# Performance work log

Measured on AMD Instinct MI355X. Metric: run time of the kernel, lower is better.

The kernel has to match this reference:

```python
import jax, jax.numpy as jnp
import numpy as np
from jax import lax

B = 512        # batch
SPEC = 300     # spectral bands / num_patches
DIM = 64
DEPTH = 5
HEADS = 4
DIM_HEAD = 16
MLP = 8
NCLS = 16
SCALE = DIM_HEAD ** -0.5


def setup_inputs() -> dict:
    key = jax.random.key(0)
    ks = jax.random.split(key, 16)
    s = 0.02
    d = {}
    d["input_tensor"] = jax.random.normal(ks[0], (B, 1, 5, 5, SPEC), jnp.float32)
    # SSE block: Conv3d(1,1,(1,1,300)) == contraction over spectral dim
    d["sse_w"] = jax.random.normal(ks[1], (SPEC,), jnp.float32) * s
    d["sse_b"] = jnp.zeros((1,), jnp.float32)
    # 3D CNN branch
    d["conv1_w"] = jax.random.normal(ks[2], (16, 1, 3, 3, 7), jnp.float32) * s
    d["conv1_b"] = jnp.zeros((16,), jnp.float32)
    d["conv2_w"] = jax.random.normal(ks[3], (32, 16, 3, 3, 3), jnp.float32) * s
    d["conv2_b"] = jnp.zeros((32,), jnp.float32)
    d["dense1_w"] = jax.random.normal(ks[4], (64, 9344), jnp.float32) * s
    d["dense1_b"] = jnp.zeros((64,), jnp.float32)
    # patch embedding + tokens
    d["patch_w"] = jax.random.normal(ks[5], (DIM, 25), jnp.float32) * s
    d["patch_b"] = jnp.zeros((DIM,), jnp.float32)
    d["cls_token"] = jax.random.normal(ks[6], (1, 1, DIM), jnp.float32)
    d["pos_emb"] = jax.random.normal(ks[7], (1, SPEC + 1, DIM), jnp.float32)
    # transformer layers (stacked over depth)
    d["ln1_g"] = jnp.ones((DEPTH, DIM), jnp.float32)
    d["ln1_b"] = jnp.zeros((DEPTH, DIM), jnp.float32)
    d["qkv_w"] = jax.random.normal(ks[8], (DEPTH, 3 * HEADS * DIM_HEAD, DIM), jnp.float32) * s
    d["attn_out_w"] = jax.random.normal(ks[9], (DEPTH, DIM, HEADS * DIM_HEAD), jnp.float32) * s
    d["attn_out_b"] = jnp.zeros((DEPTH, DIM), jnp.float32)
    d["ln2_g"] = jnp.ones((DEPTH, DIM), jnp.float32)
    d["ln2_b"] = jnp.zeros((DEPTH, DIM), jnp.float32)
    d["ff1_w"] = jax.random.normal(ks[10], (DEPTH, MLP, DIM), jnp.float32) * s
    d["ff1_b"] = jnp.zeros((DEPTH, MLP), jnp.float32)
    d["ff2_w"] = jax.random.normal(ks[11], (DEPTH, DIM, MLP), jnp.float32) * s
    d["ff2_b"] = jnp.zeros((DEPTH, DIM), jnp.float32)
    # head: LayerNorm(2*dim) + Linear(2*dim, num_classes)
    d["head_ln_g"] = jnp.ones((2 * DIM,), jnp.float32)
    d["head_ln_b"] = jnp.zeros((2 * DIM,), jnp.float32)
    d["head_w"] = jax.random.normal(ks[12], (NCLS, 2 * DIM), jnp.float32) * s
    d["head_b"] = jnp.zeros((NCLS,), jnp.float32)
    return d


def _ln(x, g, b, eps=1e-5):
    m = jnp.mean(x, -1, keepdims=True)
    v = jnp.mean((x - m) ** 2, -1, keepdims=True)
    return (x - m) * lax.rsqrt(v + eps) * g + b


def reference(input_tensor, sse_w, sse_b, conv1_w, conv1_b, conv2_w, conv2_b,
              dense1_w, dense1_b, patch_w, patch_b, cls_token, pos_emb,
              ln1_g, ln1_b, qkv_w, attn_out_w, attn_out_b, ln2_g, ln2_b,
              ff1_w, ff1_b, ff2_w, ff2_b, head_ln_g, head_ln_b, head_w, head_b):
    xin = input_tensor  # [B,1,5,5,300]
    # Spatial SE: Conv3d(1,1,(1,1,300)) -> sigmoid -> gate
    sq = jax.nn.sigmoid(jnp.einsum('bihwc,c->bhw', xin, sse_w)[:, None, :, :, None] + sse_b[0])
    xin = xin * sq

    # ---- 3D CNN branch ----
    dn = ('NCDHW', 'OIDHW', 'NCDHW')
    h = lax.conv_general_dilated(xin, conv1_w, (1, 1, 1), 'VALID', dimension_numbers=dn)
    h = jax.nn.relu(h + conv1_b[None, :, None, None, None])          # [B,16,3,3,294]
    h = lax.conv_general_dilated(h, conv2_w, (1, 1, 1), 'VALID', dimension_numbers=dn)
    h = jax.nn.relu(h + conv2_b[None, :, None, None, None])          # [B,32,1,1,292]
    y = h.reshape(h.shape[0], -1) @ dense1_w.T + dense1_b            # [B,64]

    # ---- SpectralFormer branch ----
    b = xin.shape[0]
    # torch .view(b, 1*300, 5*5) on contiguous [B,1,5,5,300]: pure C-order reshape
    x = xin.reshape(b, SPEC, 25)
    x = x @ patch_w.T + patch_b                                      # [B,300,64]
    cls = jnp.broadcast_to(cls_token, (b, 1, DIM))
    x = jnp.concatenate([cls, x], axis=1) + pos_emb[:, :SPEC + 1]    # [B,301,64]

    for i in range(DEPTH):
        # attention (residual + prenorm)
        xn = _ln(x, ln1_g[i], ln1_b[i])
        qkv = xn @ qkv_w[i].T                                        # [B,301,192]
        q, k, v = jnp.split(qkv, 3, axis=-1)
        def heads(t):
            return t.reshape(b, SPEC + 1, HEADS, DIM_HEAD).transpose(0, 2, 1, 3)
        q, k, v = heads(q), heads(k), heads(v)                       # [B,H,301,16]
        dots = jnp.einsum('bhid,bhjd->bhij', q, k) * SCALE
        attn = jax.nn.softmax(dots, axis=-1)
        o = jnp.einsum('bhij,bhjd->bhid', attn, v)
        o = o.transpose(0, 2, 1, 3).reshape(b, SPEC + 1, HEADS * DIM_HEAD)
        x = o @ attn_out_w[i].T + attn_out_b[i] + x
        # feedforward (residual + prenorm)
        xn = _ln(x, ln2_g[i], ln2_b[i])
        hid = jax.nn.gelu(xn @ ff1_w[i].T + ff1_b[i], approximate=False)
        x = hid @ ff2_w[i].T + ff2_b[i] + x

    cls_out = x[:, 0]                                                # [B,64]
    z = jnp.concatenate([cls_out, y], axis=-1)                       # [B,128]
    z = _ln(z, head_ln_g, head_ln_b)
    return z @ head_w.T + head_b                                     # [B,16]
```

## Files before the change

### kernel.cpp

```cpp
#include <hip/hip_runtime.h>
#include <cmath>

#define NB 512
#define SEQ 301
#define QSCALE 0.36067376022f

using f32x4  = __attribute__((ext_vector_type(4))) float;
using s16x4  = __attribute__((ext_vector_type(4))) short;
using s16x8  = __attribute__((ext_vector_type(8))) short;

#if __has_builtin(__builtin_amdgcn_exp2f)
#define EX2(x) __builtin_amdgcn_exp2f(x)
#else
#define EX2(x) exp2f(x)
#endif

__device__ __forceinline__ unsigned short f2bf(float f) {
  unsigned int u = __builtin_bit_cast(unsigned int, f);
  u += 0x7fffu + ((u >> 16) & 1u);
  return (unsigned short)(u >> 16);
}

__device__ __forceinline__ unsigned int pkbf(float lo, float hi) {
  unsigned int ulo = __builtin_bit_cast(unsigned int, lo) + 0x8000u;
  unsigned int uhi = __builtin_bit_cast(unsigned int, hi) + 0x8000u;
  return __builtin_amdgcn_perm(uhi, ulo, 0x07060302u);
}

__device__ __forceinline__ s16x4 pk4f(float a, float b, float c, float d) {
  uint2 u = make_uint2(pkbf(a, b), pkbf(c, d));
  return __builtin_bit_cast(s16x4, u);
}

__device__ __forceinline__ s16x4 pk4(float4 v) {
  return pk4f(v.x, v.y, v.z, v.w);
}

__device__ __forceinline__ f32x4 mm16(s16x4 a, s16x4 b, f32x4 c) {
  return __builtin_amdgcn_mfma_f32_16x16x16bf16_1k(a, b, c, 0, 0, 0);
}

__device__ __forceinline__ f32x4 mm32(s16x8 a, s16x8 b, f32x4 c) {
  return __builtin_amdgcn_mfma_f32_16x16x32_bf16(a, b, c, 0, 0, 0);
}

__device__ __forceinline__ s16x8 cat8(s16x4 a, s16x4 b) {
  return __builtin_shufflevector(a, b, 0, 1, 2, 3, 4, 5, 6, 7);
}

__device__ __forceinline__ float gelu_f(float a) {
  float z = fabsf(a) * 0.70710678f;
  float t = 1.f / (1.f + 0.3275911f * z);
  float poly = t*(0.254829592f + t*(-0.284496736f + t*(1.421413741f +
               t*(-1.453152027f + t*1.061405429f))));
  float e = EX2(-z*z*1.44269504f);
  float erfa = 1.f - poly*e;
  float erfz = copysignf(erfa, a);
  return 0.5f*a*(1.f + erfz);
}

__global__ __launch_bounds__(256) void k_prep(const float* __restrict__ w2c,
    unsigned short* __restrict__ wt2g) {
  int i = blockIdx.x*256 + threadIdx.x;
  if (i >= 96*148) return;
  int row = i/148, k = i - row*148;
  int kw_ = row >> 5, o2 = row & 31;
  unsigned short v = 0;
  if (k < 144) {
    int ci = k/9, r_ = k - ci*9;
    v = f2bf(w2c[o2*432 + ci*27 + r_*3 + kw_]);
  }
  wt2g[i] = v;
}

__global__ __launch_bounds__(256) void k_prep2(const float* __restrict__ pw,
    unsigned short* __restrict__ pwt) {
  int i = blockIdx.x*256 + threadIdx.x;
  if (i >= 64*32) return;
  int d = i >> 5, k = i & 31;
  pwt[i] = (k < 25) ? f2bf(pw[d*25 + k]) : (unsigned short)0;
}

__global__ __launch_bounds__(64) void k_sse(const float* __restrict__ xin,
    const float* __restrict__ sw, const float* __restrict__ sb, float* __restrict__ xs) {
  int blk = blockIdx.x; int b = blk / 25, p = blk % 25; int lane = threadIdx.x;
  const float* src = xin + (size_t)b*7500 + p*300;
  float s = 0.f;
  for (int c = lane; c < 300; c += 64) s += src[c]*sw[c];
  #pragma unroll
  for (int o = 32; o > 0; o >>= 1) s += __shfl_down(s, o, 64);
  s = __shfl(s, 0, 64);
  float sq = 1.f/(1.f + __expf(-(s + sb[0])));
  float* dst = xs + (size_t)b*7500 + p*300;
  for (int c = lane; c < 300; c += 64) dst[c] = src[c]*sq;
}

__global__ __launch_bounds__(256) void k_conv12(const float* __restrict__ xs,
    const float* __restrict__ w1c, const float* __restrict__ b1c,
    const unsigned short* __restrict__ wt2g, const float* __restrict__ b2c,
    float* __restrict__ c2) {
  int blk = blockIdx.x; int b = blk >> 2; int chunk = blk & 3;
  int w0 = chunk*73;
  int tid = threadIdx.x;
  int lane = tid & 63, wv = tid >> 6;
  int lm = lane & 15, lq = lane >> 4;
  __shared__ unsigned short xss[32*88];
  __shared__ unsigned short c1s[84*148];
  __shared__ alignas(8) unsigned short wt_s[96*148];

  const float* src = xs + (size_t)b*7500;
  for (int i = tid; i < 2025; i += 256) {
    int p = i/81, c = i - p*81;
    xss[p*88 + c] = f2bf(src[p*300 + w0 + c]);
  }
  for (int i = tid; i < 7*88; i += 256) xss[25*88 + i] = 0;
  for (int i = tid; i < 25*7; i += 256) { int p = i/7, c = 81 + i%7; xss[p*88 + c] = 0; }
  for (int i = tid; i < 9*148; i += 256) c1s[75*148 + i] = 0;
  {
    const uint2* wsrc = (const uint2*)wt2g;
    uint2* wdst = (uint2*)wt_s;
    for (int i = tid; i < 3552; i += 256) wdst[i] = wsrc[i];
  }

  s16x4 Af[4]; int P[4][4]; float bv[4];
  #pragma unroll
  for (int r = 0; r < 4; ++r) bv[r] = b1c[lq*4 + r];
  #pragma unroll
  for (int kc = 0; kc < 4; ++kc) {
    short e[4];
    #pragma unroll
    for (int j = 0; j < 4; ++j) {
      int k = kc*16 + lq*4 + j;
      float wf = (k < 63) ? w1c[lm*63 + k] : 0.f;
      e[j] = (short)f2bf(wf);
      int r_ = k/7, kw_ = k - r_*7;
      int kd = r_/3, kh = r_ - kd*3;
      P[kc][j] = (kd*5 + kh)*88 + kw_;
    }
    s16x4 a; a.x = e[0]; a.y = e[1]; a.z = e[2]; a.w = e[3];
    Af[kc] = a;
  }
  __syncthreads();

  for (int idx = wv; idx < 45; idx += 4) {
    int dh = idx/5, pt = idx - dh*5;
    int d0 = dh/3, h0 = dh - d0*3;
    int base = (d0*5 + h0)*88 + pt*16 + lm;
    f32x4 acc = {bv[0], bv[1], bv[2], bv[3]};
    #pragma unroll
    for (int kc = 0; kc < 4; ++kc) {
      s16x4 Bf;
      Bf.x = (short)xss[base + P[kc][0]];
      Bf.y = (short)xss[base + P[kc][1]];
      Bf.z = (short)xss[base + P[kc][2]];
      Bf.w = (short)xss[base + P[kc][3]];
      acc = mm16(Af[kc], Bf, acc);
    }
    int lw = pt*16 + lm;
    if (lw < 75) {
      unsigned short* dst = c1s + lw*148 + dh;
      #pragma unroll
      for (int r = 0; r < 4; ++r)
        dst[(lq*4 + r)*9] = f2bf(fmaxf(acc[r], 0.f));
    }
  }
  __syncthreads();

  float bvo0 = b2c[lm], bvo1 = b2c[16 + lm];
  for (int task = wv; task < 10; task += 4) {
    int pt = task >> 1, ot = task & 1;
    float bb = ot ? bvo1 : bvo0;
    f32x4 acc = {bb, bb, bb, bb};
    #pragma unroll
    for (int kw_ = 0; kw_ < 3; ++kw_) {
      int rowb = (pt*16 + lm + kw_)*148;
      int wrow = (kw_*32 + ot*16 + lm)*148;
      #pragma unroll
      for (int kc = 0; kc < 9; ++kc) {
        s16x4 Aw = *(const s16x4*)&c1s[rowb + kc*16 + lq*4];
        s16x4 Bw = *(const s16x4*)&wt_s[wrow + kc*16 + lq*4];
        acc = mm16(Aw, Bw, acc);
      }
    }
    float* dst = c2 + (size_t)b*9344 + (ot*16 + lm)*292;
    #pragma unroll
    for (int r = 0; r < 4; ++r) {
      int w2l = pt*16 + lq*4 + r;
      if (w2l < 73) dst[w0 + w2l] = fmaxf(acc[r], 0.f);
    }
  }
}

__global__ __launch_bounds__(256) void k_dense1(const float* __restrict__ c2,
    const float* __restrict__ w, float* __restrict__ part) {
  int mt = blockIdx.x & 31;
  int kc = blockIdx.x >> 5;
  int b0 = mt * 16;
  int tid = threadIdx.x;
  int lane = tid & 63; int nt = tid >> 6;
  int lm = lane & 15, lq = lane >> 4;
  int s0 = kc*36 + (kc < 8 ? kc : 8);
  int cnt = 36 + (kc < 8 ? 1 : 0);
  const float* arow = c2 + (size_t)(b0 + lm)*9344;
  const float* brow = w + (size_t)(nt*16 + lm)*9344;
  f32x4 acc = {0.f, 0.f, 0.f, 0.f};
  int koff = s0*16 + lq*4;
  #pragma unroll 4
  for (int i = 0; i < cnt; ++i, koff += 16) {
    s16x4 af = pk4(*(const float4*)(arow + koff));
    s16x4 bf = pk4(*(const float4*)(brow + koff));
    acc = mm16(af, bf, acc);
  }
  float* dst = part + (size_t)kc*32768;
  #pragma unroll
  for (int r = 0; r < 4; ++r)
    dst[(size_t)(b0 + lq*4 + r)*64 + nt*16 + lm] = acc[r];
}

__global__ __launch_bounds__(256) void k_patch(const float* __restrict__ xs,
    const unsigned short* __restrict__ pwt, const float* __restrict__ pb,
    const float* __restrict__ cls, const float* __restrict__ pos, float* __restrict__ x) {
  int b = blockIdx.x;
  int tid = threadIdx.x;
  int lane = tid & 63; int nt = tid >> 6;
  int lm = lane & 15, lq = lane >> 4;
  __shared__ unsigned short P_s[304*36];

  const float* src = xs + (size_t)b*7500;
  for (int i = tid; i < 304*32; i += 256) {
    int row = i >> 5, k = i & 31;
    unsigned short v = 0;
    if (row >= 1 && row <= 300 && k < 25) v = f2bf(src[(row-1)*25 + k]);
    P_s[row*36 + k] = v;
  }
  __syncthreads();

  int d = nt*16 + lm;
  s16x4 Bf0 = *(const s16x4*)&pwt[d*32 + lq*4];
  s16x4 Bf1 = *(const s16x4*)&pwt[d*32 + 16 + lq*4];
  float pbd = pb[d];
  float clsd = cls[d];
  for (int rt = 0; rt < 19; ++rt) {
    const unsigned short* prow = &P_s[(rt*16 + lm)*36];
    s16x4 A0 = *(const s16x4*)&prow[lq*4];
    s16x4 A1 = *(const s16x4*)&prow[16 + lq*4];
    f32x4 acc = {0.f,0.f,0.f,0.f};
    acc = mm16(A0, Bf0, acc);
    acc = mm16(A1, Bf1, acc);
    #pragma unroll
    for (int r = 0; r < 4; ++r) {
      int t = rt*16 + lq*4 + r;
      if (t < SEQ) {
        float val = acc[r] + pbd + pos[t*64 + d];
        if (t == 0) val = clsd + pos[d];
        x[((size_t)b*SEQ + t)*64 + d] = val;
      }
    }
  }
}

__global__ __launch_bounds__(256) void k_layer(float* __restrict__ x,
    const float* __restrict__ g, const float* __restrict__ bt,
    const float* __restrict__ qkvw, unsigned short* __restrict__ ao,
    const float* __restrict__ w, const float* __restrict__ bias,
    const float* __restrict__ g2, const float* __restrict__ bt2,
    const float* __restrict__ w1, const float* __restrict__ b1,
    const float* __restrict__ w2, const float* __restrict__ b2) {
  int b = blockIdx.x;
  int tid = threadIdx.x;
  int lane = tid & 63, h = tid >> 6;
  int lm = lane & 15, lq = lane >> 4;
  __shared__ unsigned short xn_s[304*68];

  for (int rr = tid; rr < 304; rr += 256) {
    int src = rr < 301 ? rr : 300;
    const float4* xp = (const float4*)(x + ((size_t)b*SEQ + src)*64);
    float4 xv[16];
    #pragma unroll
    for (int i = 0; i < 16; ++i) xv[i] = xp[i];
    float m = 0.f;
    #pragma unroll
    for (int i = 0; i < 16; ++i) m += xv[i].x + xv[i].y + xv[i].z + xv[i].w;
    m *= (1.f/64.f);
    float var = 0.f;
    #pragma unroll
    for (int i = 0; i < 16; ++i) {
      float a = xv[i].x-m, bb = xv[i].y-m, c = xv[i].z-m, dd = xv[i].w-m;
      var += a*a + bb*bb + c*c + dd*dd;
    }
    float rs = rsqrtf(var*(1.f/64.f) + 1e-5f);
    const float4* g4 = (const float4*)g;
    const float4* b4 = (const float4*)bt;
    #pragma unroll
    for (int i = 0; i < 16; ++i) {
      float4 gg = g4[i]; float4 bb = b4[i];
      float e0 = (xv[i].x-m)*rs*gg.x + bb.x;
      float e1 = (xv[i].y-m)*rs*gg.y + bb.y;
      float e2 = (xv[i].z-m)*rs*gg.z + bb.z;
      float e3 = (xv[i].w-m)*rs*gg.w + bb.w;
      *(uint2*)&xn_s[rr*68 + i*4] = make_uint2(pkbf(e0, e1), pkbf(e2, e3));
    }
  }

  s16x4 WqA[4], WkA[4], WvB[4];
  #pragma unroll
  for (int c = 0; c < 4; ++c) {
    float4 wq = *(const float4*)(qkvw + (size_t)(h*16 + lm)*64 + c*16 + lq*4);
    WqA[c] = pk4f(wq.x*QSCALE, wq.y*QSCALE, wq.z*QSCALE, wq.w*QSCALE);
    WkA[c] = pk4(*(const float4*)(qkvw + (size_t)(64 + h*16 + lm)*64 + c*16 + lq*4));
    WvB[c] = pk4(*(const float4*)(qkvw + (size_t)(128 + h*16 + lm)*64 + c*16 + lq*4));
  }
  __syncthreads();

  s16x4 Kreg[19], Vreg[19];
  #pragma unroll
  for (int rt = 0; rt < 19; ++rt) {
    s16x4 Af[4];
    #pragma unroll
    for (int c = 0; c < 4; ++c)
      Af[c] = *(const s16x4*)&xn_s[(rt*16 + lm)*68 + c*16 + lq*4];
    f32x4 aK = {0.f,0.f,0.f,0.f}, aV = {0.f,0.f,0.f,0.f};
    #pragma unroll
    for (int c = 0; c < 4; ++c) {
      aK = mm16(WkA[c], Af[c], aK);
      aV = mm16(Af[c], WvB[c], aV);
    }
    Kreg[rt] = pk4f(aK[0], aK[1], aK[2], aK[3]);
    Vreg[rt] = pk4f(aV[0], aV[1], aV[2], aV[3]);
  }

  for (int pi = 0; pi < 10; ++pi) {
    int qt0 = 2*pi;
    int qt1 = 2*pi + 1;
    bool two = (qt1 < 19);
    int qt1c = two ? qt1 : qt0;
    s16x4 qb0, qb1;
    {
      s16x4 Af0[4], Af1[4];
      #pragma unroll
      for (int c = 0; c < 4; ++c) {
        Af0[c] = *(const s16x4*)&xn_s[(qt0*16 + lm)*68 + c*16 + lq*4];
        Af1[c] = *(const s16x4*)&xn_s[(qt1c*16 + lm)*68 + c*16 + lq*4];
      }
      f32x4 a0 = {0.f,0.f,0.f,0.f}, a1 = {0.f,0.f,0.f,0.f};
      #pragma unroll
      for (int c = 0; c < 4; ++c) {
        a0 = mm16(WqA[c], Af0[c], a0);
        a1 = mm16(WqA[c], Af1[c], a1);
      }
      qb0 = pk4f(a0[0], a0[1], a0[2], a0[3]);
      qb1 = pk4f(a1[0], a1[1], a1[2], a1[3]);
    }
    f32x4 o0 = {0.f,0.f,0.f,0.f}, o1 = {0.f,0.f,0.f,0.f};
    float l0 = 0.f, l1 = 0.f;
    #pragma unroll
    for (int t = 0; t < 9; ++t) {
      s16x4 kaa = Kreg[2*t];
      s16x4 kab = Kreg[2*t + 1];
      s16x8 vb = cat8(Vreg[2*t], Vreg[2*t + 1]);
      f32x4 z = {0.f,0.f,0.f,0.f};
      f32x4 s0a = mm16(kaa, qb0, z);
      f32x4 s0b = mm16(kab, qb0, z);
      f32x4 s1a = mm16(kaa, qb1, z);
      f32x4 s1b = mm16(kab, qb1, z);
      float p00 = EX2(s0a[0]), p01 = EX2(s0a[1]), p02 = EX2(s0a[2]), p03 = EX2(s0a[3]);
      float p04 = EX2(s0b[0]), p05 = EX2(s0b[1]), p06 = EX2(s0b[2]), p07 = EX2(s0b[3]);
      float p10 = EX2(s1a[0]), p11 = EX2(s1a[1]), p12 = EX2(s1a[2]), p13 = EX2(s1a[3]);
      float p14 = EX2(s1b[0]), p15 = EX2(s1b[1]), p16 = EX2(s1b[2]), p17 = EX2(s1b[3]);
      l0 += ((p00 + p01) + (p02 + p03)) + ((p04 + p05) + (p06 + p07));
      l1 += ((p10 + p11) + (p12 + p13)) + ((p14 + p15) + (p16 + p17));
      s16x8 pa0 = cat8(pk4f(p00, p01, p02, p03), pk4f(p04, p05, p06, p07));
      s16x8 pa1 = cat8(pk4f(p10, p11, p12, p13), pk4f(p14, p15, p16, p17));
      o0 = mm32(pa0, vb, o0);
      o1 = mm32(pa1, vb, o1);
    }
    {
      s16x4 ka = Kreg[18];
      s16x4 vb = Vreg[18];
      f32x4 z = {0.f,0.f,0.f,0.f};
      f32x4 st0 = mm16(ka, qb0, z);
      f32x4 st1 = mm16(ka, qb1, z);
      int kbase = 288 + lq*4;
      float p00 = (kbase + 0 < SEQ) ? EX2(st0[0]) : 0.f;
      float p01 = (kbase + 1 < SEQ) ? EX2(st0[1]) : 0.f;
      float p02 = (kbase + 2 < SEQ) ? EX2(st0[2]) : 0.f;
      float p03 = (kbase + 3 < SEQ) ? EX2(st0[3]) : 0.f;
      float p10 = (kbase + 0 < SEQ) ? EX2(st1[0]) : 0.f;
      float p11 = (kbase + 1 < SEQ) ? EX2(st1[1]) : 0.f;
      float p12 = (kbase + 2 < SEQ) ? EX2(st1[2]) : 0.f;
      float p13 = (kbase + 3 < SEQ) ? EX2(st1[3]) : 0.f;
      l0 += (p00 + p01) + (p02 + p03);
      l1 += (p10 + p11) + (p12 + p13);
      s16x4 pa0 = pk4f(p00, p01, p02, p03);
      s16x4 pa1 = pk4f(p10, p11, p12, p13);
      o0 = mm16(pa0, vb, o0);
      o1 = mm16(pa1, vb, o1);
    }
    l0 += __shfl_xor(l0, 16, 64); l0 += __shfl_xor(l0, 32, 64);
    l1 += __shfl_xor(l1, 16, 64); l1 += __shfl_xor(l1, 32, 64);
    float li0 = 1.f / l0;
    float li1 = 1.f / l1;
    #pragma unroll
    for (int r = 0; r < 4; ++r) {
      int q0 = qt0*16 + lq*4 + r;
      float lr0 = __shfl(li0, lq*4 + r, 64);
      if (q0 < SEQ) ao[((size_t)b*SEQ + q0)*64 + h*16 + lm] = f2bf(o0[r] * lr0);
      if (two) {
        int q1 = qt1*16 + lq*4 + r;
        float lr1 = __shfl(li1, lq*4 + r, 64);
        if (q1 < SEQ) ao[((size_t)b*SEQ + q1)*64 + h*16 + lm] = f2bf(o1[r] * lr1);
      }
    }
  }
  __syncthreads();
#if __has_builtin(__builtin_amdgcn_sched_barrier)
  __builtin_amdgcn_sched_barrier(0);
#endif

  {
    s16x4 Bf[4][4];
    #pragma unroll
    for (int nt = 0; nt < 4; ++nt) {
      #pragma unroll
      for (int c = 0; c < 4; ++c) {
        float4 wf = *(const float4*)(w + (size_t)(nt*16 + lm)*64 + c*16 + lq*4);
        Bf[nt][c] = pk4(wf);
      }
    }
    float biasv[4], gv[4], btv[4], b2v[4];
    float w1r[8][4], w2r[4][8];
    float b1v[8];
    #pragma unroll
    for (int nt = 0; nt < 4; ++nt) {
      biasv[nt] = bias[nt*16 + lm];
      gv[nt]    = g2[nt*16 + lm];
      btv[nt]   = bt2[nt*16 + lm];
      b2v[nt]   = b2[nt*16 + lm];
      #pragma unroll
      for (int t = 0; t < 8; ++t) w2r[nt][t] = w2[(nt*16 + lm)*8 + t];
    }
    #pragma unroll
    for (int t = 0; t < 8; ++t) {
      b1v[t] = b1[t];
      #pragma unroll
      for (int nt = 0; nt < 4; ++nt) w1r[t][nt] = w1[t*64 + nt*16 + lm];
    }

    for (int rt = h; rt < 19; rt += 4) {
      int rsrc = rt*16 + lm; if (rsrc > 300) rsrc = 300;
      const unsigned short* arow = ao + ((size_t)b*SEQ + rsrc)*64;
      int row0 = rt*16 + lq*4;
      float xpre[4][4];
      #pragma unroll
      for (int r = 0; r < 4; ++r) {
        int row = row0 + r; int rs2 = row > 300 ? 300 : row;
        const float* xr = x + ((size_t)b*SEQ + rs2)*64;
        #pragma unroll
        for (int nt = 0; nt < 4; ++nt) xpre[r][nt] = xr[nt*16 + lm];
      }
      f32x4 acc[4];
      #pragma unroll
      for (int nt = 0; nt < 4; ++nt)
        acc[nt] = (f32x4){biasv[nt], biasv[nt], biasv[nt], biasv[nt]};
      #pragma unroll
      for (int c = 0; c < 4; ++c) {
        s16x4 af = *(const s16x4*)(arow + c*16 + lq*4);
        #pragma unroll
        for (int nt = 0; nt < 4; ++nt) acc[nt] = mm16(af, Bf[nt][c], acc[nt]);
      }
      float v[4][4];
      #pragma unroll
      for (int r = 0; r < 4; ++r)
        #pragma unroll
        for (int nt = 0; nt < 4; ++nt) v[r][nt] = acc[nt][r] + xpre[r][nt];
      #pragma unroll
      for (int r = 0; r < 4; ++r) {
        float s = (v[r][0] + v[r][1]) + (v[r][2] + v[r][3]);
        s += __shfl_xor(s, 1, 64); s += __shfl_xor(s, 2, 64);
        s += __shfl_xor(s, 4, 64); s += __shfl_xor(s, 8, 64);
        float m = s * (1.f/64.f);
        float c0 = v[r][0]-m, c1 = v[r][1]-m, c2 = v[r][2]-m, c3 = v[r][3]-m;
        float s2 = (c0*c0 + c1*c1) + (c2*c2 + c3*c3);
        s2 += __shfl_xor(s2, 1, 64); s2 += __shfl_xor(s2, 2, 64);
        s2 += __shfl_xor(s2, 4, 64); s2 += __shfl_xor(s2, 8, 64);
        float rs = rsqrtf(s2*(1.f/64.f) + 1e-5f);
        float xn0 = c0*rs*gv[0] + btv[0];
        float xn1 = c1*rs*gv[1] + btv[1];
        float xn2 = c2*rs*gv[2] + btv[2];
        float xn3 = c3*rs*gv[3] + btv[3];
        float hg[8];
        #pragma unroll
        for (int t = 0; t < 8; ++t) {
          float p = xn0*w1r[t][0] + xn1*w1r[t][1] + xn2*w1r[t][2] + xn3*w1r[t][3];
          p += __shfl_xor(p, 1, 64); p += __shfl_xor(p, 2, 64);
          p += __shfl_xor(p, 4, 64); p += __shfl_xor(p, 8, 64);
          hg[t] = gelu_f(p + b1v[t]);
        }
        int row = row0 + r;
        if (row < SEQ) {
          float* xw = x + ((size_t)b*SEQ + row)*64;
          #pragma unroll
          for (int nt = 0; nt < 4; ++nt) {
            float o = 0.f;
            #pragma unroll
            for (int t = 0; t < 8; ++t) o += hg[t]*w2r[nt][t];
            xw[nt*16 + lm] = v[r][nt] + o + b2v[nt];
          }
        }
      }
    }
  }
}

__global__ __launch_bounds__(128) void k_head(const float* __restrict__ x,
    const float* __restrict__ part, const float* __restrict__ d1b,
    const float* __restrict__ g, const float* __restrict__ bt,
    const float* __restrict__ hw, const float* __restrict__ hb, float* __restrict__ out) {
  int b = blockIdx.x; int t = threadIdx.x; int lane = t & 63; int wv = t >> 6;
  float v;
  if (t < 64) {
    v = x[(size_t)b*SEQ*64 + t];
  } else {
    int o = t - 64;
    float acc = d1b[o];
    #pragma unroll
    for (int kc = 0; kc < 16; ++kc) acc += part[(size_t)kc*32768 + b*64 + o];
    v = acc;
  }
  __shared__ float rbuf[2];
  __shared__ float z_s[128];
  float s = v;
  #pragma unroll
  for (int o = 32; o; o >>= 1) s += __shfl_down(s, o, 64);
  if (lane == 0) rbuf[wv] = s;
  __syncthreads();
  float m = (rbuf[0] + rbuf[1]) * (1.f/128.f);
  __syncthreads();
  float c = v - m;
  float s2 = c*c;
  #pragma unroll
  for (int o = 32; o; o >>= 1) s2 += __shfl_down(s2, o, 64);
  if (lane == 0) rbuf[wv] = s2;
  __syncthreads();
  float var = (rbuf[0] + rbuf[1]) * (1.f/128.f);
  z_s[t] = c * rsqrtf(var + 1e-5f) * g[t] + bt[t];
  __syncthreads();
  if (t < 16) {
    float a = hb[t];
    const float* wr = hw + t*128;
    #pragma unroll 8
    for (int j = 0; j < 128; ++j) a += z_s[j]*wr[j];
    out[(size_t)b*16 + t] = a;
  }
}

extern "C" void kernel_launch(void* const* d_in, const int* in_sizes, int n_in,
                              void* d_out, int out_size, void* d_ws, size_t ws_size,
                              hipStream_t stream) {
  const float* input      = (const float*)d_in[0];
  const float* sse_w      = (const float*)d_in[1];
  const float* sse_b      = (const float*)d_in[2];
  const float* conv1_w    = (const float*)d_in[3];
  const float* conv1_b    = (const float*)d_in[4];
  const float* conv2_w    = (const float*)d_in[5];
  const float* conv2_b    = (const float*)d_in[6];
  const float* dense1_w   = (const float*)d_in[7];
  const float* dense1_b   = (const float*)d_in[8];
  const float* patch_w    = (const float*)d_in[9];
  const float* patch_b    = (const float*)d_in[10];
  const float* cls_token  = (const float*)d_in[11];
  const float* pos_emb    = (const float*)d_in[12];
  const float* ln1_g      = (const float*)d_in[13];
  const float* ln1_b      = (const float*)d_in[14];
  const float* qkv_w      = (const float*)d_in[15];
  const float* attn_out_w = (const float*)d_in[16];
  const float* attn_out_b = (const float*)d_in[17];
  const float* ln2_g      = (const float*)d_in[18];
  const float* ln2_b      = (const float*)d_in[19];
  const float* ff1_w      = (const float*)d_in[20];
  const float* ff1_b      = (const float*)d_in[21];
  const float* ff2_w      = (const float*)d_in[22];
  const float* ff2_b      = (const float*)d_in[23];
  const float* head_ln_g  = (const float*)d_in[24];
  const float* head_ln_b  = (const float*)d_in[25];
  const float* head_w     = (const float*)d_in[26];
  const float* head_b     = (const float*)d_in[27];
  float* out = (float*)d_out;

  float* ws = (float*)d_ws;
  float* xs  = ws;
  float* part = ws;
  float* y   = xs + 3840000;
  unsigned short* wt2g = (unsigned short*)y;
  unsigned short* pwt  = (unsigned short*)(y + 16384);
  float* x   = y + 32768;
  float* R   = x + 9863168;
  float* c2  = R + 21676032;
  unsigned short* ao = (unsigned short*)R;

  k_prep  <<<56, 256, 0, stream>>>(conv2_w, wt2g);
  k_prep2 <<<8, 256, 0, stream>>>(patch_w, pwt);
  k_sse   <<<NB*25, 64, 0, stream>>>(input, sse_w, sse_b, xs);
  k_conv12<<<NB*4, 256, 0, stream>>>(xs, conv1_w, conv1_b, wt2g, conv2_b, c2);
  k_patch <<<NB, 256, 0, stream>>>(xs, pwt, patch_b, cls_token, pos_emb, x);
  k_dense1<<<512, 256, 0, stream>>>(c2, dense1_w, part);
  for (int i = 0; i < 5; ++i) {
    k_layer<<<NB, 256, 0, stream>>>(x, ln1_g + i*64, ln1_b + i*64,
                 qkv_w + (size_t)i*192*64, ao,
                 attn_out_w + (size_t)i*4096, attn_out_b + i*64,
                 ln2_g + i*64, ln2_b + i*64,
                 ff1_w + (size_t)i*512, ff1_b + i*8, ff2_w + (size_t)i*512, ff2_b + i*64);
  }
  k_head<<<NB, 128, 0, stream>>>(x, part, dense1_b, head_ln_g, head_ln_b, head_w, head_b, out);
}
```

Measured before the change: 664.8 us.

## Keep attention output in LDS, precompute Q, process four query tiles

Q is now computed for all row tiles together with K and V and held in registers, and after a barrier the attention loop handles four query tiles per iteration instead of two. The normalized attention output goes into the existing shared xn_s buffer rather than a global bf16 scratch array, and the out-projection reads it from there. This removes a global write/read round trip and reuses K/V fragments across more queries, but adds 19 more register fragments and more live accumulators, which raises register pressure and can cause spills or lower occupancy.

```diff
diff --git a/kernel.cpp b/kernel.cpp
--- a/kernel.cpp
+++ b/kernel.cpp
@@ -261,7 +261,7 @@
 
 __global__ __launch_bounds__(256) void k_layer(float* __restrict__ x,
     const float* __restrict__ g, const float* __restrict__ bt,
-    const float* __restrict__ qkvw, unsigned short* __restrict__ ao,
+    const float* __restrict__ qkvw,
     const float* __restrict__ w, const float* __restrict__ bias,
     const float* __restrict__ g2, const float* __restrict__ bt2,
     const float* __restrict__ w1, const float* __restrict__ b1,
@@ -312,103 +312,84 @@
   }
   __syncthreads();
 
-  s16x4 Kreg[19], Vreg[19];
+  s16x4 Kreg[19], Vreg[19], Qreg[19];
   #pragma unroll
   for (int rt = 0; rt < 19; ++rt) {
     s16x4 Af[4];
     #pragma unroll
     for (int c = 0; c < 4; ++c)
       Af[c] = *(const s16x4*)&xn_s[(rt*16 + lm)*68 + c*16 + lq*4];
-    f32x4 aK = {0.f,0.f,0.f,0.f}, aV = {0.f,0.f,0.f,0.f};
+    f32x4 aK = {0.f,0.f,0.f,0.f}, aV = {0.f,0.f,0.f,0.f}, aQ = {0.f,0.f,0.f,0.f};
     #pragma unroll
     for (int c = 0; c < 4; ++c) {
       aK = mm16(WkA[c], Af[c], aK);
       aV = mm16(Af[c], WvB[c], aV);
+      aQ = mm16(WqA[c], Af[c], aQ);
     }
     Kreg[rt] = pk4f(aK[0], aK[1], aK[2], aK[3]);
     Vreg[rt] = pk4f(aV[0], aV[1], aV[2], aV[3]);
-  }
-
-  for (int pi = 0; pi < 10; ++pi) {
-    int qt0 = 2*pi;
-    int qt1 = 2*pi + 1;
-    bool two = (qt1 < 19);
-    int qt1c = two ? qt1 : qt0;
-    s16x4 qb0, qb1;
-    {
-      s16x4 Af0[4], Af1[4];
-      #pragma unroll
-      for (int c = 0; c < 4; ++c) {
-        Af0[c] = *(const s16x4*)&xn_s[(qt0*16 + lm)*68 + c*16 + lq*4];
-        Af1[c] = *(const s16x4*)&xn_s[(qt1c*16 + lm)*68 + c*16 + lq*4];
-      }
-      f32x4 a0 = {0.f,0.f,0.f,0.f}, a1 = {0.f,0.f,0.f,0.f};
-      #pragma unroll
-      for (int c = 0; c < 4; ++c) {
-        a0 = mm16(WqA[c], Af0[c], a0);
-        a1 = mm16(WqA[c], Af1[c], a1);
-      }
-      qb0 = pk4f(a0[0], a0[1], a0[2], a0[3]);
-      qb1 = pk4f(a1[0], a1[1], a1[2], a1[3]);
-    }
-    f32x4 o0 = {0.f,0.f,0.f,0.f}, o1 = {0.f,0.f,0.f,0.f};
-    float l0 = 0.f, l1 = 0.f;
+    Qreg[rt] = pk4f(aQ[0], aQ[1], aQ[2], aQ[3]);
+  }
+  __syncthreads();
+
+  for (int pi = 0; pi < 5; ++pi) {
+    int qt[4]; bool act[4];
+    s16x4 qb[4];
+    #pragma unroll
+    for (int c = 0; c < 4; ++c) {
+      int q = pi*4 + c;
+      act[c] = (q < 19);
+      qt[c] = act[c] ? q : 18;
+      qb[c] = Qreg[qt[c]];
+    }
+    f32x4 o_[4];
+    float l_[4];
+    #pragma unroll
+    for (int c = 0; c < 4; ++c) { o_[c] = (f32x4){0.f,0.f,0.f,0.f}; l_[c] = 0.f; }
     #pragma unroll
     for (int t = 0; t < 9; ++t) {
       s16x4 kaa = Kreg[2*t];
       s16x4 kab = Kreg[2*t + 1];
       s16x8 vb = cat8(Vreg[2*t], Vreg[2*t + 1]);
-      f32x4 z = {0.f,0.f,0.f,0.f};
-      f32x4 s0a = mm16(kaa, qb0, z);
-      f32x4 s0b = mm16(kab, qb0, z);
-      f32x4 s1a = mm16(kaa, qb1, z);
-      f32x4 s1b = mm16(kab, qb1, z);
-      float p00 = EX2(s0a[0]), p01 = EX2(s0a[1]), p02 = EX2(s0a[2]), p03 = EX2(s0a[3]);
-      float p04 = EX2(s0b[0]), p05 = EX2(s0b[1]), p06 = EX2(s0b[2]), p07 = EX2(s0b[3]);
-      float p10 = EX2(s1a[0]), p11 = EX2(s1a[1]), p12 = EX2(s1a[2]), p13 = EX2(s1a[3]);
-      float p14 = EX2(s1b[0]), p15 = EX2(s1b[1]), p16 = EX2(s1b[2]), p17 = EX2(s1b[3]);
-      l0 += ((p00 + p01) + (p02 + p03)) + ((p04 + p05) + (p06 + p07));
-      l1 += ((p10 + p11) + (p12 + p13)) + ((p14 + p15) + (p16 + p17));
-      s16x8 pa0 = cat8(pk4f(p00, p01, p02, p03), pk4f(p04, p05, p06, p07));
-      s16x8 pa1 = cat8(pk4f(p10, p11, p12, p13), pk4f(p14, p15, p16, p17));
-      o0 = mm32(pa0, vb, o0);
-      o1 = mm32(pa1, vb, o1);
+      #pragma unroll
+      for (int c = 0; c < 4; ++c) {
+        f32x4 z = {0.f,0.f,0.f,0.f};
+        f32x4 sa = mm16(kaa, qb[c], z);
+        f32x4 sb = mm16(kab, qb[c], z);
+        float p0 = EX2(sa[0]), p1 = EX2(sa[1]), p2 = EX2(sa[2]), p3 = EX2(sa[3]);
+        float p4 = EX2(sb[0]), p5 = EX2(sb[1]), p6 = EX2(sb[2]), p7 = EX2(sb[3]);
+        l_[c] += ((p0 + p1) + (p2 + p3)) + ((p4 + p5) + (p6 + p7));
+        s16x8 pa = cat8(pk4f(p0, p1, p2, p3), pk4f(p4, p5, p6, p7));
+        o_[c] = mm32(pa, vb, o_[c]);
+      }
     }
     {
       s16x4 ka = Kreg[18];
-      s16x4 vb = Vreg[18];
-      f32x4 z = {0.f,0.f,0.f,0.f};
-      f32x4 st0 = mm16(ka, qb0, z);
-      f32x4 st1 = mm16(ka, qb1, z);
+      s16x4 vb4 = Vreg[18];
       int kbase = 288 + lq*4;
-      float p00 = (kbase + 0 < SEQ) ? EX2(st0[0]) : 0.f;
-      float p01 = (kbase + 1 < SEQ) ? EX2(st0[1]) : 0.f;
-      float p02 = (kbase + 2 < SEQ) ? EX2(st0[2]) : 0.f;
-      float p03 = (kbase + 3 < SEQ) ? EX2(st0[3]) : 0.f;
-      float p10 = (kbase + 0 < SEQ) ? EX2(st1[0]) : 0.f;
-      float p11 = (kbase + 1 < SEQ) ? EX2(st1[1]) : 0.f;
-      float p12 = (kbase + 2 < SEQ) ? EX2(st1[2]) : 0.f;
-      float p13 = (kbase + 3 < SEQ) ? EX2(st1[3]) : 0.f;
-      l0 += (p00 + p01) + (p02 + p03);
-      l1 += (p10 + p11) + (p12 + p13);
-      s16x4 pa0 = pk4f(p00, p01, p02, p03);
-      s16x4 pa1 = pk4f(p10, p11, p12, p13);
-      o0 = mm16(pa0, vb, o0);
-      o1 = mm16(pa1, vb, o1);
-    }
-    l0 += __shfl_xor(l0, 16, 64); l0 += __shfl_xor(l0, 32, 64);
-    l1 += __shfl_xor(l1, 16, 64); l1 += __shfl_xor(l1, 32, 64);
-    float li0 = 1.f / l0;
-    float li1 = 1.f / l1;
-    #pragma unroll
-    for (int r = 0; r < 4; ++r) {
-      int q0 = qt0*16 + lq*4 + r;
-      float lr0 = __shfl(li0, lq*4 + r, 64);
-      if (q0 < SEQ) ao[((size_t)b*SEQ + q0)*64 + h*16 + lm] = f2bf(o0[r] * lr0);
-      if (two) {
-        int q1 = qt1*16 + lq*4 + r;
-        float lr1 = __shfl(li1, lq*4 + r, 64);
-        if (q1 < SEQ) ao[((size_t)b*SEQ + q1)*64 + h*16 + lm] = f2bf(o1[r] * lr1);
+      #pragma unroll
+      for (int c = 0; c < 4; ++c) {
+        f32x4 z = {0.f,0.f,0.f,0.f};
+        f32x4 st = mm16(ka, qb[c], z);
+        float p0 = (kbase + 0 < SEQ) ? EX2(st[0]) : 0.f;
+        float p1 = (kbase + 1 < SEQ) ? EX2(st[1]) : 0.f;
+        float p2 = (kbase + 2 < SEQ) ? EX2(st[2]) : 0.f;
+        float p3 = (kbase + 3 < SEQ) ? EX2(st[3]) : 0.f;
+        l_[c] += (p0 + p1) + (p2 + p3);
+        o_[c] = mm16(pk4f(p0, p1, p2, p3), vb4, o_[c]);
+      }
+    }
+    #pragma unroll
+    for (int c = 0; c < 4; ++c) {
+      float l = l_[c];
+      l += __shfl_xor(l, 16, 64); l += __shfl_xor(l, 32, 64);
+      float li = 1.f / l;
+      #pragma unroll
+      for (int r = 0; r < 4; ++r) {
+        int q = qt[c]*16 + lq*4 + r;
+        float lr = __shfl(li, lq*4 + r, 64);
+        if (act[c] && q < SEQ)
+          xn_s[q*68 + h*16 + lm] = f2bf(o_[c][r] * lr);
       }
     }
   }
@@ -448,7 +429,7 @@
 
     for (int rt = h; rt < 19; rt += 4) {
       int rsrc = rt*16 + lm; if (rsrc > 300) rsrc = 300;
-      const unsigned short* arow = ao + ((size_t)b*SEQ + rsrc)*64;
+      const unsigned short* arow = &xn_s[rsrc*68];
       int row0 = rt*16 + lq*4;
       float xpre[4][4];
       #pragma unroll
@@ -596,7 +577,6 @@
   float* x   = y + 32768;
   float* R   = x + 9863168;
   float* c2  = R + 21676032;
-  unsigned short* ao = (unsigned short*)R;
 
   k_prep  <<<56, 256, 0, stream>>>(conv2_w, wt2g);
   k_prep2 <<<8, 256, 0, stream>>>(patch_w, pwt);
@@ -606,7 +586,7 @@
   k_dense1<<<512, 256, 0, stream>>>(c2, dense1_w, part);
   for (int i = 0; i < 5; ++i) {
     k_layer<<<NB, 256, 0, stream>>>(x, ln1_g + i*64, ln1_b + i*64,
-                 qkv_w + (size_t)i*192*64, ao,
+                 qkv_w + (size_t)i*192*64,
                  attn_out_w + (size_t)i*4096, attn_out_b + i*64,
                  ln2_g + i*64, ln2_b + i*64,
                  ff1_w + (size_t)i*512, ff1_b + i*8, ff2_w + (size_t)i*512, ff2_b + i*64);
```

Result: slower. 685.9 us (+3.2%).
